# Kernel tuning notes

Measured on AMD Instinct MI355X. Metric: run time of the kernel, lower is better.

Reference implementation:

```python
import jax, jax.numpy as jnp
import numpy as np

B, N, DIM = 4, 4096, 512
H, DH, M, ITERS = 8, 64, 256, 6
KW = 33  # residual conv kernel length (along seq)


def setup_inputs() -> dict:
    key = jax.random.key(0)
    k1, k2, k3, k4 = jax.random.split(key, 4)
    return {
        "x": jax.random.normal(k1, (B, N, DIM), dtype=jnp.float32),
        "Wqkv": jax.random.normal(k2, (DIM, 3 * H * DH), dtype=jnp.float32) * 0.02,
        "Wout": jax.random.normal(k3, (H * DH, DIM), dtype=jnp.float32) * 0.02,
        "bout": jnp.zeros((DIM,), dtype=jnp.float32),
        "res_kernel": jax.random.normal(k4, (H, 1, KW, 1), dtype=jnp.float32) * 0.1,
    }


def _pinv_iter(x):
    # Moore-Penrose iterative pseudo-inverse, 6 Newton-Schulz-like steps.
    col = jnp.abs(x).sum(-1)  # ... i
    row = jnp.abs(x).sum(-2)  # ... j
    z = jnp.swapaxes(x, -1, -2) / (jnp.max(col) * jnp.max(row))
    I = jnp.eye(x.shape[-1], dtype=x.dtype)
    for _ in range(ITERS):
        xz = x @ z
        z = 0.25 * z @ (13.0 * I - xz @ (15.0 * I - xz @ (7.0 * I - xz)))
    return z


def reference(x, Wqkv, Wout, bout, res_kernel):
    b, n, _ = x.shape
    l = n // M  # landmark pooling window (n divisible by M -> no padding branch)
    scale = DH ** -0.5

    qkv = x @ Wqkv  # [b, n, 3*h*dh]
    q, k, v = jnp.split(qkv, 3, axis=-1)
    to_bhnd = lambda t: t.reshape(b, n, H, DH).transpose(0, 2, 1, 3)
    q, k, v = to_bhnd(q), to_bhnd(k), to_bhnd(v)
    q = q * scale

    # landmarks: mean over contiguous windows of size l
    q_lm = q.reshape(b, H, M, l, DH).sum(3) / l  # [b,h,m,dh]
    k_lm = k.reshape(b, H, M, l, DH).sum(3) / l

    sim1 = jnp.einsum('bhid,bhjd->bhij', q, k_lm)     # [b,h,n,m]
    sim2 = jnp.einsum('bhid,bhjd->bhij', q_lm, k_lm)  # [b,h,m,m]
    sim3 = jnp.einsum('bhid,bhjd->bhij', q_lm, k)     # [b,h,m,n]

    attn1 = jax.nn.softmax(sim1, axis=-1)
    attn2 = jax.nn.softmax(sim2, axis=-1)
    attn3 = jax.nn.softmax(sim3, axis=-1)

    attn2_inv = _pinv_iter(attn2)
    out = (attn1 @ attn2_inv) @ (attn3 @ v)  # [b,h,n,dh]

    # depthwise residual conv along the sequence axis of v
    pad = KW // 2
    conv = jax.lax.conv_general_dilated(
        v, res_kernel,
        window_strides=(1, 1),
        padding=((pad, pad), (0, 0)),
        dimension_numbers=('NCHW', 'OIHW', 'NCHW'),
        feature_group_count=H,
    )
    out = out + conv

    out = out.transpose(0, 2, 1, 3).reshape(b, n, H * DH)
    return out @ Wout + bout
```

## Files before the change

### kernel.cpp

```cpp
#include <hip/hip_runtime.h>
#include <math.h>

constexpr int BATCH = 4;
constexpr int SEQ   = 4096;
constexpr int DIMC  = 512;
constexpr int NH    = 8;
constexpr int HD    = 64;
constexpr int NLM   = 256;
constexpr int LWIN  = 16;
constexpr int KWIN  = 33;
constexpr int BH    = BATCH * NH;

typedef __attribute__((ext_vector_type(8))) short  bfrag;
typedef __attribute__((ext_vector_type(4))) float  ffrag;
typedef __attribute__((ext_vector_type(8))) unsigned short us8;
typedef __attribute__((ext_vector_type(4))) unsigned short us4;
typedef unsigned short ush;

__device__ __forceinline__ ush f2bf(float f) {
  unsigned u = __builtin_bit_cast(unsigned, f);
  return (ush)((u + 0x7FFFu + ((u >> 16) & 1u)) >> 16);
}
__device__ __forceinline__ float bf2f(ush h) {
  unsigned u = ((unsigned)h) << 16;
  return __builtin_bit_cast(float, u);
}
__device__ __forceinline__ void splitf(float f, ush& h, ush& l) {
  h = f2bf(f);
  l = f2bf(f - bf2f(h));
}
__device__ __forceinline__ void gl_lds16(const ush* g, ush* l) {
  __builtin_amdgcn_global_load_lds(
      (const __attribute__((address_space(1))) void*)g,
      (__attribute__((address_space(3))) void*)l, 16, 0, 0);
}

__global__ void split_flat(const float* __restrict__ src, ush* __restrict__ oh,
                           ush* __restrict__ ol, int n4) {
  for (int i = blockIdx.x * 256 + threadIdx.x; i < n4; i += gridDim.x * 256) {
    float4 f = ((const float4*)src)[i];
    us4 h, l;
    float fs[4] = {f.x, f.y, f.z, f.w};
#pragma unroll
    for (int j = 0; j < 4; ++j) {
      ush hh, ll;
      splitf(fs[j], hh, ll);
      h[j] = hh; l[j] = ll;
    }
    ((us4*)oh)[i] = h;
    ((us4*)ol)[i] = l;
  }
}

__global__ __launch_bounds__(256) void transpose_split_w(const float* __restrict__ in,
                                                         ush* __restrict__ oh,
                                                         ush* __restrict__ ol,
                                                         int R, int C) {
  __shared__ float T[32][33];
  const int tid = threadIdx.x;
  const int c0 = blockIdx.x * 32, r0 = blockIdx.y * 32;
#pragma unroll
  for (int u = 0; u < 4; ++u) {
    int r = (tid >> 5) * 4 + u, cl = tid & 31;
    T[r][cl] = in[(size_t)(r0 + r) * C + c0 + cl];
  }
  __syncthreads();
#pragma unroll
  for (int u = 0; u < 4; ++u) {
    int cl = (tid >> 5) * 4 + u, rl = tid & 31;
    float f = T[rl][cl];
    ush h, l; splitf(f, h, l);
    size_t o = (size_t)(c0 + cl) * R + r0 + rl;
    oh[o] = h; ol[o] = l;
  }
}

__global__ __launch_bounds__(256) void qkv_mfma(const ush* __restrict__ xh,
                                                const ush* __restrict__ xl,
                                                const ush* __restrict__ wTh,
                                                ush* __restrict__ q_bf,
                                                ush* __restrict__ k_bf,
                                                ush* __restrict__ vT,
                                                float* __restrict__ qlm,
                                                float* __restrict__ klm) {
  __shared__ ush Ash[128][40], Asl[128][40];
  __shared__ ush Bsh[128][40];
  const int tid = threadIdx.x;
  const int w = tid >> 6, lane = tid & 63;
  const int lm = lane & 15, lq = lane >> 4;
  const int wm = w >> 1, wn = w & 1;
  const int row0 = blockIdx.x * 128, col0 = blockIdx.y * 128;
  const ffrag fz = {0.f, 0.f, 0.f, 0.f};
  ffrag acc[4][4];
#pragma unroll
  for (int i = 0; i < 4; ++i)
#pragma unroll
    for (int j = 0; j < 4; ++j) acc[i][j] = fz;

  const int sm = tid >> 1, skoff = (tid & 1) * 16;
  for (int k0 = 0; k0 < 512; k0 += 32) {
    __syncthreads();
    {
      size_t ao = (size_t)(row0 + sm) * 512 + k0 + skoff;
      *(us8*)&Ash[sm][skoff]     = *(const us8*)&xh[ao];
      *(us8*)&Ash[sm][skoff + 8] = *(const us8*)&xh[ao + 8];
      *(us8*)&Asl[sm][skoff]     = *(const us8*)&xl[ao];
      *(us8*)&Asl[sm][skoff + 8] = *(const us8*)&xl[ao + 8];
      size_t bo = (size_t)(col0 + sm) * 512 + k0 + skoff;
      *(us8*)&Bsh[sm][skoff]     = *(const us8*)&wTh[bo];
      *(us8*)&Bsh[sm][skoff + 8] = *(const us8*)&wTh[bo + 8];
    }
    __syncthreads();
    bfrag ah[4], al[4], bh[4];
#pragma unroll
    for (int mt = 0; mt < 4; ++mt) {
      ah[mt] = *(const bfrag*)&Ash[64 * wm + 16 * mt + lm][8 * lq];
      al[mt] = *(const bfrag*)&Asl[64 * wm + 16 * mt + lm][8 * lq];
    }
#pragma unroll
    for (int nt = 0; nt < 4; ++nt)
      bh[nt] = *(const bfrag*)&Bsh[64 * wn + 16 * nt + lm][8 * lq];
#pragma unroll
    for (int mt = 0; mt < 4; ++mt)
#pragma unroll
      for (int nt = 0; nt < 4; ++nt) {
        acc[mt][nt] = __builtin_amdgcn_mfma_f32_16x16x32_bf16(ah[mt], bh[nt], acc[mt][nt], 0, 0, 0);
        acc[mt][nt] = __builtin_amdgcn_mfma_f32_16x16x32_bf16(al[mt], bh[nt], acc[mt][nt], 0, 0, 0);
      }
  }
#pragma unroll
  for (int mt = 0; mt < 4; ++mt) {
    int rbase = row0 + 64 * wm + 16 * mt;
    int b = rbase >> 12;
    int ntok_base = rbase & 4095;
    int win = ntok_base >> 4;
#pragma unroll
    for (int nt = 0; nt < 4; ++nt) {
      int n_local = 64 * wn + 16 * nt;
      int col = col0 + n_local + lm;
      int which = col >> 9;
      int h = (col >> 6) & 7;
      int d = col & 63;
      int bh_i = b * NH + h;
      float scale = (which == 0) ? 0.125f : 1.0f;
      float vals[4];
      float s = 0.f;
#pragma unroll
      for (int r = 0; r < 4; ++r) {
        vals[r] = acc[mt][nt][r] * scale;
        s += vals[r];
      }
      if (which == 2) {
        ush* dst = &vT[((size_t)bh_i * HD + d) * SEQ + ntok_base + 4 * lq];
#pragma unroll
        for (int r = 0; r < 4; ++r) dst[r] = f2bf(vals[r]);
      } else {
        ush* dst = which == 0 ? q_bf : k_bf;
#pragma unroll
        for (int r = 0; r < 4; ++r) {
          int ntok = ntok_base + 4 * lq + r;
          dst[((size_t)bh_i * SEQ + ntok) * HD + d] = f2bf(vals[r]);
        }
        s += __shfl_xor(s, 16);
        s += __shfl_xor(s, 32);
        if (lq == 0) {
          float* lmdst = which == 0 ? qlm : klm;
          lmdst[((size_t)bh_i * NLM + win) * HD + d] = s * (1.0f / LWIN);
        }
      }
    }
  }
}

__global__ __launch_bounds__(256) void sim2_softmax(const float* __restrict__ qlm,
                                                    const float* __restrict__ klm,
                                                    ush* __restrict__ a2h,
                                                    ush* __restrict__ a2l) {
  int i = blockIdx.x & 255;
  int bh = blockIdx.x >> 8;
  int j = threadIdx.x;
  __shared__ float qrow[64];
  __shared__ float red[256];
  if (j < 64) qrow[j] = qlm[((size_t)bh * NLM + i) * HD + j];
  __syncthreads();
  const float* kr = klm + ((size_t)bh * NLM + j) * HD;
  float s = 0.f;
#pragma unroll
  for (int d = 0; d < 64; d += 4) {
    float4 kv = *(const float4*)&kr[d];
    s += qrow[d] * kv.x + qrow[d + 1] * kv.y + qrow[d + 2] * kv.z + qrow[d + 3] * kv.w;
  }
  red[j] = s; __syncthreads();
  for (int off = 128; off > 0; off >>= 1) {
    if (j < off) red[j] = fmaxf(red[j], red[j + off]);
    __syncthreads();
  }
  float mx = red[0]; __syncthreads();
  float e = expf(s - mx);
  red[j] = e; __syncthreads();
  for (int off = 128; off > 0; off >>= 1) {
    if (j < off) red[j] += red[j + off];
    __syncthreads();
  }
  float val = e / red[0];
  size_t o = ((size_t)bh * NLM + i) * NLM + j;
  ush h, l; splitf(val, h, l);
  a2h[o] = h; a2l[o] = l;
}

__global__ __launch_bounds__(256) void colmax(const ush* __restrict__ a2h,
                                              float* __restrict__ red) {
  int bh = blockIdx.x;
  int t = threadIdx.x;
  const size_t base = (size_t)bh * NLM * NLM;
  float cs = 0.f;
  for (int i = 0; i < NLM; ++i) cs += bf2f(a2h[base + (size_t)i * NLM + t]);
  __shared__ float r1[256];
  r1[t] = cs; __syncthreads();
  for (int off = 128; off > 0; off >>= 1) {
    if (t < off) r1[t] = fmaxf(r1[t], r1[t + off]);
    __syncthreads();
  }
  if (t == 0) red[bh] = r1[0];
}

__global__ void finalize_scale(float* __restrict__ red) {
  if (threadIdx.x == 0) {
    float m1 = -1e30f;
    for (int i = 0; i < BH; ++i) m1 = fmaxf(m1, red[i]);
    red[64] = 1.0f / m1;
  }
}

__global__ __launch_bounds__(256) void zinit_split(const ush* __restrict__ a2h,
                                                   const ush* __restrict__ a2l,
                                                   const float* __restrict__ red,
                                                   ush* __restrict__ zAh, ush* __restrict__ zAl,
                                                   ush* __restrict__ zBh, ush* __restrict__ zBl) {
  __shared__ float T[32][33];
  const int tid = threadIdx.x;
  const int bh = blockIdx.z;
  const int j0 = blockIdx.x * 32, i0 = blockIdx.y * 32;
  const float s = red[64];
  const size_t base = (size_t)bh * NLM * NLM;
#pragma unroll
  for (int u = 0; u < 4; ++u) {
    int jl = (tid >> 5) * 4 + u, il = tid & 31;
    size_t o = base + (size_t)(j0 + jl) * NLM + i0 + il;
    float a = (bf2f(a2h[o]) + bf2f(a2l[o])) * s;
    T[jl][il] = a;
    ush h, l; splitf(a, h, l);
    zBh[o] = h; zBl[o] = l;
  }
  __syncthreads();
#pragma unroll
  for (int u = 0; u < 4; ++u) {
    int il = (tid >> 5) * 4 + u, jl = tid & 31;
    float a = T[jl][il];
    ush h, l; splitf(a, h, l);
    size_t o = base + (size_t)(i0 + il) * NLM + j0 + jl;
    zAh[o] = h; zAl[o] = l;
  }
}

__device__ __forceinline__ void stage_gemm(
    ush (*S)[2][8][64][8],
    const ush* Ah, const ush* Al, const ush* Bh, const ush* Bl,
    const ush* E1h, const ush* E1l, const ush* E2h, const ush* E2l,
    ush* oAh, ush* oAl, ush* oBh, ush* oBl,
    int M, int N, int K, float alpha, float beta, float coef,
    int bx, int by, int batch, int tid) {
  const size_t abase = (size_t)batch * M * K;
  const size_t bbase = (size_t)batch * N * K;
  const size_t ebase = (size_t)batch * M * N;
  const int w = tid >> 6, lane = tid & 63;
  const int lm = lane & 15, lq = lane >> 4;
  const int wm = w >> 1, wn = w & 1;
  const int row0 = bx * 64, col0 = by * 64;
  const bool uAl = (Al != nullptr);
  const bool uBl = (Bl != nullptr);
  const ffrag fz = {0.f, 0.f, 0.f, 0.f};
  ffrag acc[2][2] = {{fz, fz}, {fz, fz}};

  const size_t arow = abase + (size_t)(row0 + lane) * K;
  const size_t brow = bbase + (size_t)(col0 + lane) * K;

  for (int k0 = 0; k0 < K; k0 += 64) {
    __syncthreads();
#pragma unroll
    for (int ci = 0; ci < 2; ++ci) {
      int c = 2 * w + ci;
      gl_lds16(&Ah[arow + k0 + 8 * c], &S[0][0][c][0][0]);
      gl_lds16(&Bh[brow + k0 + 8 * c], &S[1][0][c][0][0]);
      if (uAl) gl_lds16(&Al[arow + k0 + 8 * c], &S[0][1][c][0][0]);
      if (uBl) gl_lds16(&Bl[brow + k0 + 8 * c], &S[1][1][c][0][0]);
    }
    __syncthreads();
#pragma unroll
    for (int ks = 0; ks < 2; ++ks) {
      bfrag ah[2], al[2], bhf[2], blf[2];
#pragma unroll
      for (int mt = 0; mt < 2; ++mt) {
        ah[mt] = *(const bfrag*)&S[0][0][4 * ks + lq][32 * wm + 16 * mt + lm][0];
        if (uAl) al[mt] = *(const bfrag*)&S[0][1][4 * ks + lq][32 * wm + 16 * mt + lm][0];
      }
#pragma unroll
      for (int nt = 0; nt < 2; ++nt) {
        bhf[nt] = *(const bfrag*)&S[1][0][4 * ks + lq][32 * wn + 16 * nt + lm][0];
        if (uBl) blf[nt] = *(const bfrag*)&S[1][1][4 * ks + lq][32 * wn + 16 * nt + lm][0];
      }
#pragma unroll
      for (int mt = 0; mt < 2; ++mt)
#pragma unroll
        for (int nt = 0; nt < 2; ++nt) {
          acc[mt][nt] = __builtin_amdgcn_mfma_f32_16x16x32_bf16(ah[mt], bhf[nt], acc[mt][nt], 0, 0, 0);
          if (uAl) acc[mt][nt] = __builtin_amdgcn_mfma_f32_16x16x32_bf16(al[mt], bhf[nt], acc[mt][nt], 0, 0, 0);
          if (uBl) acc[mt][nt] = __builtin_amdgcn_mfma_f32_16x16x32_bf16(ah[mt], blf[nt], acc[mt][nt], 0, 0, 0);
        }
    }
  }
#pragma unroll
  for (int mt = 0; mt < 2; ++mt)
#pragma unroll
    for (int nt = 0; nt < 2; ++nt) {
      int n = col0 + 32 * wn + 16 * nt + lm;
#pragma unroll
      for (int r = 0; r < 4; ++r) {
        int m = row0 + 32 * wm + 16 * mt + 4 * lq + r;
        float c = acc[mt][nt][r];
        float e = 0.f;
        size_t eo = ebase + (size_t)m * N + n;
        if (E1h) {
          float t = bf2f(E1h[eo]);
          if (E1l) t += bf2f(E1l[eo]);
          e += alpha * t;
        }
        if (E2h) {
          float t = bf2f(E2h[eo]);
          if (E2l) t += bf2f(E2l[eo]);
          e += beta * t;
        }
        float y = coef * (e - c);
        ush h, l; splitf(y, h, l);
        if (oAh) {
          size_t o = ebase + (size_t)m * N + n;
          oAh[o] = h;
          if (oAl) oAl[o] = l;
        }
        if (oBh) {
          size_t o = (size_t)batch * N * M + (size_t)n * M + m;
          oBh[o] = h;
          if (oBl) oBl[o] = l;
        }
      }
    }
}

__global__ __launch_bounds__(256) void bgemm_split(
    const ush* Ah, const ush* Al, const ush* Bh, const ush* Bl,
    const ush* E1h, const ush* E1l, const ush* E2h, const ush* E2l,
    ush* oAh, ush* oAl, ush* oBh, ush* oBl,
    int M, int N, int K, float alpha, float beta, float coef) {
  __shared__ ush S[2][2][8][64][8];
  stage_gemm(S, Ah, Al, Bh, Bl, E1h, E1l, E2h, E2l, oAh, oAl, oBh, oBl,
             M, N, K, alpha, beta, coef, blockIdx.x, blockIdx.y, blockIdx.z,
             threadIdx.x);
}

__global__ __launch_bounds__(256) void ns_s2(
    const ush* Yh, const ush* Yl, const ush* zh, const ush* zl,
    ush* t2h, ush* t2l, ush* Uh, ush* Ul) {
  __shared__ ush S[2][2][8][64][8];
  const int bz = blockIdx.z, batch = bz >> 1;
  if ((bz & 1) == 0) {
    stage_gemm(S, Yh, Yl, Yh, Yl, Yh, Yl, nullptr, nullptr,
               t2h, t2l, nullptr, nullptr,
               256, 256, 256, 7.f, 0.f, 1.f,
               blockIdx.x, blockIdx.y, batch, threadIdx.x);
  } else {
    stage_gemm(S, zh, zl, Yh, Yl, nullptr, nullptr, nullptr, nullptr,
               Uh, Ul, nullptr, nullptr,
               256, 256, 256, 0.f, 0.f, -1.f,
               blockIdx.x, blockIdx.y, batch, threadIdx.x);
  }
}

constexpr int NCH = 4;
__global__ __launch_bounds__(256) void sim3_mfma(const float* __restrict__ qlm,
                                                 const ush* __restrict__ k_bf,
                                                 const ush* __restrict__ vT_bf,
                                                 float* __restrict__ O_part,
                                                 float* __restrict__ l_part) {
  constexpr int CHUNK = SEQ / NCH;
  __shared__ ush Qs[64][72];
  __shared__ ush Ks[128][72];
  __shared__ ush Vs[64][136];
  __shared__ ush Ps[64][136];
  const int bh = blockIdx.z;
  const int m0 = blockIdx.x * 64;
  const int n_base = blockIdx.y * CHUNK;
  const int tid = threadIdx.x;
  const int w = tid >> 6, lane = tid & 63;
  const int lm = lane & 15, lq = lane >> 4;
  {
    int m = tid >> 2, off = (tid & 3) * 16;
    const float* src = &qlm[((size_t)bh * NLM + m0 + m) * HD + off];
    us8 o0, o1;
#pragma unroll
    for (int j = 0; j < 8; ++j) o0[j] = f2bf(src[j]);
#pragma unroll
    for (int j = 0; j < 8; ++j) o1[j] = f2bf(src[8 + j]);
    *(us8*)&Qs[m][off] = o0;
    *(us8*)&Qs[m][off + 8] = o1;
  }
  const ffrag fz = {0.f, 0.f, 0.f, 0.f};
  ffrag O[4] = {fz, fz, fz, fz};
  float lsum[4] = {0.f, 0.f, 0.f, 0.f};

  for (int n0 = 0; n0 < CHUNK; n0 += 128) {
    __syncthreads();
    {
      int n = tid >> 1, off = (tid & 1) * 32;
      const ush* src = &k_bf[((size_t)bh * SEQ + n_base + n0 + n) * HD + off];
#pragma unroll
      for (int u = 0; u < 4; ++u) *(us8*)&Ks[n][off + 8 * u] = *(const us8*)&src[8 * u];
    }
    {
      int d = tid >> 2, off = (tid & 3) * 32;
      const ush* src = &vT_bf[((size_t)bh * HD + d) * SEQ + n_base + n0 + off];
#pragma unroll
      for (int u = 0; u < 4; ++u) *(us8*)&Vs[d][off + 8 * u] = *(const us8*)&src[8 * u];
    }
    __syncthreads();
    ffrag S[8] = {fz, fz, fz, fz, fz, fz, fz, fz};
#pragma unroll
    for (int ks = 0; ks < 2; ++ks) {
      bfrag a = *(const bfrag*)&Qs[16 * w + lm][32 * ks + 8 * lq];
#pragma unroll
      for (int t = 0; t < 8; ++t) {
        bfrag b = *(const bfrag*)&Ks[16 * t + lm][32 * ks + 8 * lq];
        S[t] = __builtin_amdgcn_mfma_f32_16x16x32_bf16(a, b, S[t], 0, 0, 0);
      }
    }
#pragma unroll
    for (int t = 0; t < 8; ++t)
#pragma unroll
      for (int r = 0; r < 4; ++r) {
        float p = __expf(S[t][r]);
        lsum[r] += p;
        Ps[16 * w + 4 * lq + r][16 * t + lm] = f2bf(p);
      }
    __syncthreads();
#pragma unroll
    for (int kk = 0; kk < 4; ++kk) {
      bfrag a = *(const bfrag*)&Ps[16 * w + lm][32 * kk + 8 * lq];
#pragma unroll
      for (int t2 = 0; t2 < 4; ++t2) {
        bfrag b = *(const bfrag*)&Vs[16 * t2 + lm][32 * kk + 8 * lq];
        O[t2] = __builtin_amdgcn_mfma_f32_16x16x32_bf16(a, b, O[t2], 0, 0, 0);
      }
    }
  }
#pragma unroll
  for (int r = 0; r < 4; ++r) {
#pragma unroll
    for (int off = 1; off < 16; off <<= 1) lsum[r] += __shfl_xor(lsum[r], off);
  }
  const size_t pbase = (size_t)blockIdx.y * 32 + bh;
  if (lm == 0) {
#pragma unroll
    for (int r = 0; r < 4; ++r)
      l_part[pbase * NLM + m0 + 16 * w + 4 * lq + r] = lsum[r];
  }
#pragma unroll
  for (int t2 = 0; t2 < 4; ++t2)
#pragma unroll
    for (int r = 0; r < 4; ++r) {
      int m = m0 + 16 * w + 4 * lq + r;
      int d = 16 * t2 + lm;
      O_part[(pbase * NLM + m) * HD + d] = O[t2][r];
    }
}

__global__ __launch_bounds__(256) void sim3_finalize(const float* __restrict__ O_part,
                                                     const float* __restrict__ l_part,
                                                     ush* __restrict__ svBh,
                                                     ush* __restrict__ svBl) {
  __shared__ float T[128][17];
  __shared__ float ls[128];
  const int bh = blockIdx.y;
  const int d0 = (blockIdx.x & 3) * 16;
  const int m0 = (blockIdx.x >> 2) * 128;
  const int tid = threadIdx.x;
  if (tid < 128) {
    float s = 0.f;
#pragma unroll
    for (int c = 0; c < NCH; ++c) s += l_part[(size_t)(c * 32 + bh) * NLM + m0 + tid];
    ls[tid] = s;
  }
#pragma unroll
  for (int i = 0; i < 8; ++i) {
    int e = i * 256 + tid;
    int m = e >> 4, dd = e & 15;
    float s = 0.f;
#pragma unroll
    for (int c = 0; c < NCH; ++c)
      s += O_part[(((size_t)(c * 32 + bh)) << 14) + (size_t)(m0 + m) * HD + d0 + dd];
    T[m][dd] = s;
  }
  __syncthreads();
#pragma unroll
  for (int i = 0; i < 8; ++i) {
    int e = i * 256 + tid;
    int dd = e >> 7, m = e & 127;
    float val = T[m][dd] / ls[m];
    ush h, l; splitf(val, h, l);
    size_t o = ((size_t)bh * HD + d0 + dd) * NLM + m0 + m;
    svBh[o] = h; svBl[o] = l;
  }
}

__global__ __launch_bounds__(256) void attn1_mfma(const ush* __restrict__ q_bf,
                                                  const float* __restrict__ klm,
                                                  const ush* __restrict__ ttT,
                                                  float* __restrict__ outp) {
  __shared__ ush bufA[256 * 72];
  __shared__ ush bufB[64 * 264];
  const int bh = blockIdx.y;
  const int b = bh >> 3, h = bh & 7;
  const int i0 = blockIdx.x * 64;
  const int tid = threadIdx.x;
  const int w = tid >> 6, lane = tid & 63;
  const int lm = lane & 15, lq = lane >> 4;
  {
    int m = tid >> 2, off = (tid & 3) * 16;
    const ush* src = &q_bf[((size_t)bh * SEQ + i0 + m) * HD + off];
    *(us8*)&bufB[m * 72 + off] = *(const us8*)src;
    *(us8*)&bufB[m * 72 + off + 8] = *(const us8*)&src[8];
  }
  {
    const float* kb = klm + (size_t)bh * NLM * HD;
#pragma unroll
    for (int u = 0; u < 16; ++u) {
      int e4 = u * 256 + tid;
      float4 f = ((const float4*)kb)[e4];
      int row = e4 >> 4, col = (e4 & 15) * 4;
      ush* p = &bufA[row * 72 + col];
      p[0] = f2bf(f.x); p[1] = f2bf(f.y); p[2] = f2bf(f.z); p[3] = f2bf(f.w);
    }
  }
  __syncthreads();
  const ffrag fz = {0.f, 0.f, 0.f, 0.f};
  ffrag S[16];
#pragma unroll
  for (int t = 0; t < 16; ++t) S[t] = fz;
#pragma unroll
  for (int ks = 0; ks < 2; ++ks) {
    bfrag a = *(const bfrag*)&bufB[(16 * w + lm) * 72 + 32 * ks + 8 * lq];
#pragma unroll
    for (int t = 0; t < 16; ++t) {
      bfrag bb = *(const bfrag*)&bufA[(16 * t + lm) * 72 + 32 * ks + 8 * lq];
      S[t] = __builtin_amdgcn_mfma_f32_16x16x32_bf16(a, bb, S[t], 0, 0, 0);
    }
  }
  float rinv[4];
  float ev[16][4];
#pragma unroll
  for (int r = 0; r < 4; ++r) {
    float mx = -INFINITY;
#pragma unroll
    for (int t = 0; t < 16; ++t) mx = fmaxf(mx, S[t][r]);
#pragma unroll
    for (int off = 1; off < 16; off <<= 1) mx = fmaxf(mx, __shfl_xor(mx, off));
    float sm = 0.f;
#pragma unroll
    for (int t = 0; t < 16; ++t) { ev[t][r] = __expf(S[t][r] - mx); sm += ev[t][r]; }
#pragma unroll
    for (int off = 1; off < 16; off <<= 1) sm += __shfl_xor(sm, off);
    rinv[r] = 1.0f / sm;
  }
  __syncthreads();
#pragma unroll
  for (int t = 0; t < 16; ++t)
#pragma unroll
    for (int r = 0; r < 4; ++r)
      bufB[(16 * w + 4 * lq + r) * 264 + 16 * t + lm] = f2bf(ev[t][r]);
  {
    const ush* tb = ttT + (size_t)bh * HD * NLM;
#pragma unroll
    for (int u = 0; u < 8; ++u) {
      int e8 = u * 256 + tid;
      int row = e8 >> 5, col = (e8 & 31) * 8;
      *(us8*)&bufA[row * 264 + col] = *(const us8*)&tb[row * NLM + col];
    }
  }
  __syncthreads();
  ffrag O[4] = {fz, fz, fz, fz};
#pragma unroll
  for (int kk = 0; kk < 8; ++kk) {
    bfrag a = *(const bfrag*)&bufB[(16 * w + lm) * 264 + 32 * kk + 8 * lq];
#pragma unroll
    for (int t2 = 0; t2 < 4; ++t2) {
      bfrag bb = *(const bfrag*)&bufA[(16 * t2 + lm) * 264 + 32 * kk + 8 * lq];
      O[t2] = __builtin_amdgcn_mfma_f32_16x16x32_bf16(a, bb, O[t2], 0, 0, 0);
    }
  }
#pragma unroll
  for (int t2 = 0; t2 < 4; ++t2)
#pragma unroll
    for (int r = 0; r < 4; ++r) {
      int i = i0 + 16 * w + 4 * lq + r;
      int d = 16 * t2 + lm;
      outp[((size_t)b * SEQ + i) * DIMC + h * HD + d] = O[t2][r] * rinv[r];
    }
}

__global__ __launch_bounds__(256) void conv_add_split(const float* __restrict__ outp,
                                                      const ush* __restrict__ vT,
                                                      const float* __restrict__ kern,
                                                      ush* __restrict__ oh,
                                                      ush* __restrict__ ol) {
  __shared__ float vt[64 * 97];
  __shared__ float ks[KWIN];
  const int bh = blockIdx.y;
  const int b = bh >> 3, hh = bh & 7;
  const int n0 = blockIdx.x * 64;
  const int tid = threadIdx.x;
  if (tid < KWIN) ks[tid] = kern[hh * KWIN + tid];
  for (int e = tid; e < 64 * 96; e += 256) {
    int d = e / 96, c = e % 96;
    int n = n0 - 16 + c;
    vt[d * 97 + c] = (n >= 0 && n < SEQ) ? bf2f(vT[((size_t)bh * HD + d) * SEQ + n]) : 0.f;
  }
  __syncthreads();
  const int d = tid & 63, g = tid >> 6;
  float wreg[48];
#pragma unroll
  for (int j = 0; j < 48; ++j) wreg[j] = vt[d * 97 + g * 16 + j];
#pragma unroll
  for (int nn = 0; nn < 16; ++nn) {
    float s = 0.f;
#pragma unroll
    for (int t = 0; t < KWIN; ++t) s = fmaf(ks[t], wreg[nn + t], s);
    int n = n0 + g * 16 + nn;
    size_t o = ((size_t)b * SEQ + n) * DIMC + hh * HD + d;
    float val = outp[o] + s;
    ush h, l; splitf(val, h, l);
    oh[o] = h; ol[o] = l;
  }
}

__global__ __launch_bounds__(256) void out_gemm_split(const ush* __restrict__ ah_g,
                                                      const ush* __restrict__ al_g,
                                                      const ush* __restrict__ bh_g,
                                                      const ush* __restrict__ bl_g,
                                                      const float* __restrict__ bias,
                                                      float* __restrict__ out) {
  __shared__ ush Ash[128][40], Asl[128][40];
  __shared__ ush Bsh[128][40], Bsl[128][40];
  const int tid = threadIdx.x;
  const int w = tid >> 6, lane = tid & 63;
  const int lm = lane & 15, lq = lane >> 4;
  const int wm = w >> 1, wn = w & 1;
  const int row0 = blockIdx.x * 128, col0 = blockIdx.y * 128;
  const ffrag fz = {0.f, 0.f, 0.f, 0.f};
  ffrag acc[4][4];
#pragma unroll
  for (int i = 0; i < 4; ++i)
#pragma unroll
    for (int j = 0; j < 4; ++j) acc[i][j] = fz;

  const int sm = tid >> 1, skoff = (tid & 1) * 16;
  for (int k0 = 0; k0 < 512; k0 += 32) {
    __syncthreads();
    {
      size_t ao = (size_t)(row0 + sm) * 512 + k0 + skoff;
      *(us8*)&Ash[sm][skoff]     = *(const us8*)&ah_g[ao];
      *(us8*)&Ash[sm][skoff + 8] = *(const us8*)&ah_g[ao + 8];
      *(us8*)&Asl[sm][skoff]     = *(const us8*)&al_g[ao];
      *(us8*)&Asl[sm][skoff + 8] = *(const us8*)&al_g[ao + 8];
      size_t bo = (size_t)(col0 + sm) * 512 + k0 + skoff;
      *(us8*)&Bsh[sm][skoff]     = *(const us8*)&bh_g[bo];
      *(us8*)&Bsh[sm][skoff + 8] = *(const us8*)&bh_g[bo + 8];
      *(us8*)&Bsl[sm][skoff]     = *(const us8*)&bl_g[bo];
      *(us8*)&Bsl[sm][skoff + 8] = *(const us8*)&bl_g[bo + 8];
    }
    __syncthreads();
    bfrag ah[4], al[4], bh[4], bl[4];
#pragma unroll
    for (int mt = 0; mt < 4; ++mt) {
      ah[mt] = *(const bfrag*)&Ash[64 * wm + 16 * mt + lm][8 * lq];
      al[mt] = *(const bfrag*)&Asl[64 * wm + 16 * mt + lm][8 * lq];
    }
#pragma unroll
    for (int nt = 0; nt < 4; ++nt) {
      bh[nt] = *(const bfrag*)&Bsh[64 * wn + 16 * nt + lm][8 * lq];
      bl[nt] = *(const bfrag*)&Bsl[64 * wn + 16 * nt + lm][8 * lq];
    }
#pragma unroll
    for (int mt = 0; mt < 4; ++mt)
#pragma unroll
      for (int nt = 0; nt < 4; ++nt) {
        acc[mt][nt] = __builtin_amdgcn_mfma_f32_16x16x32_bf16(ah[mt], bh[nt], acc[mt][nt], 0, 0, 0);
        acc[mt][nt] = __builtin_amdgcn_mfma_f32_16x16x32_bf16(al[mt], bh[nt], acc[mt][nt], 0, 0, 0);
        acc[mt][nt] = __builtin_amdgcn_mfma_f32_16x16x32_bf16(ah[mt], bl[nt], acc[mt][nt], 0, 0, 0);
      }
  }
#pragma unroll
  for (int mt = 0; mt < 4; ++mt)
#pragma unroll
    for (int nt = 0; nt < 4; ++nt) {
      int n = col0 + 64 * wn + 16 * nt + lm;
      float bv = bias[n];
#pragma unroll
      for (int r = 0; r < 4; ++r) {
        int m = row0 + 64 * wm + 16 * mt + 4 * lq + r;
        out[(size_t)m * 512 + n] = acc[mt][nt][r] + bv;
      }
    }
}

extern "C" void kernel_launch(void* const* d_in, const int* in_sizes, int n_in,
                              void* d_out, int out_size, void* d_ws, size_t ws_size,
                              hipStream_t stream) {
  const float* x    = (const float*)d_in[0];
  const float* Wqkv = (const float*)d_in[1];
  const float* Wout = (const float*)d_in[2];
  const float* bout = (const float*)d_in[3];
  const float* rker = (const float*)d_in[4];
  float* out = (float*)d_out;
  float* ws = (float*)d_ws;

  ush*   vT     = (ush*)(ws);
  ush*   q_bf   = (ush*)(ws + 4194304);
  float* regA   = ws + 8388608;
  float* regB   = ws + 16777216;
  float* qlm    = ws + 25165824;
  float* klm    = ws + 25690112;
  float* regC   = ws + 26214400;
  float* a2reg  = ws + 28311552;
  float* zAreg  = ws + 30408704;
  float* zBreg  = ws + 34603008;
  float* xzreg  = ws + 38797312;
  float* t3reg  = ws + 43515904;
  float* wqkvT  = ws + 45613056;
  float* woutT  = ws + 46399488;
  float* red    = ws + 46661632;

  ush* k_bf  = (ush*)regA;
  float* outp = regA;
  ush* xh = (ush*)regB;
  ush* xl = (ush*)(regB + 4194304);
  ush* outph = (ush*)regB;
  ush* outpl = (ush*)(regB + 4194304);
  ush* a2h = (ush*)a2reg;
  ush* a2l = (ush*)(a2reg + 1048576);
  ush* zA_[4] = {(ush*)zAreg, (ush*)(zAreg + 1048576), (ush*)(zAreg + 2097152), (ush*)(zAreg + 3145728)};
  ush* zB_[4] = {(ush*)zBreg, (ush*)(zBreg + 1048576), (ush*)(zBreg + 2097152), (ush*)(zBreg + 3145728)};
  ush* Y_h  = (ush*)xzreg;
  ush* Y_l  = (ush*)(xzreg + 1048576);
  ush* t2_h = (ush*)regC;
  ush* t2_l = (ush*)(regC + 1048576);
  ush* U_h  = (ush*)t3reg;
  ush* U_l  = (ush*)(t3reg + 1048576);
  float* O_part = xzreg;
  float* l_part = xzreg + 2097152;
  ush* svB_h = (ush*)t3reg;
  ush* svB_l = (ush*)(t3reg + 262144);
  ush* ttT   = (ush*)regC;
  ush* wqkvT_h = (ush*)wqkvT;
  ush* wqkvT_l = (ush*)(wqkvT + 393216);
  ush* woutT_h = (ush*)woutT;
  ush* woutT_l = (ush*)(woutT + 131072);

  split_flat<<<2048, 256, 0, stream>>>(x, xh, xl, 2097152);
  transpose_split_w<<<dim3(48, 16), 256, 0, stream>>>(Wqkv, wqkvT_h, wqkvT_l, 512, 1536);
  transpose_split_w<<<dim3(16, 16), 256, 0, stream>>>(Wout, woutT_h, woutT_l, 512, 512);

  qkv_mfma<<<dim3(128, 12), 256, 0, stream>>>(xh, xl, wqkvT_h,
                                              q_bf, k_bf, vT, qlm, klm);

  sim2_softmax<<<8192, 256, 0, stream>>>(qlm, klm, a2h, a2l);
  colmax<<<32, 256, 0, stream>>>(a2h, red);
  finalize_scale<<<1, 64, 0, stream>>>(red);
  zinit_split<<<dim3(8, 8, 32), 256, 0, stream>>>(a2h, a2l, red,
                                                  zA_[0], zA_[1], zA_[2], zA_[3]);

  ush** zc = zA_;
  ush** zn = zB_;
  for (int it = 0; it < 6; ++it) {
    const bool zin_s  = (it == 5);
    const bool a2_s   = (it >= 4);
    const bool mid_s  = (it >= 4);
    const bool zout_s = (it >= 4);
    bgemm_split<<<dim3(4, 4, 32), 256, 0, stream>>>(
        a2h, a2_s ? a2l : nullptr,
        zc[2], zin_s ? zc[3] : nullptr,
        nullptr, nullptr, nullptr, nullptr,
        Y_h, mid_s ? Y_l : nullptr, nullptr, nullptr,
        256, 256, 256, 0.f, 0.f, -1.f);
    ns_s2<<<dim3(4, 4, 64), 256, 0, stream>>>(
        Y_h, mid_s ? Y_l : nullptr,
        zc[0], zin_s ? zc[1] : nullptr,
        t2_h, mid_s ? t2_l : nullptr,
        U_h, mid_s ? U_l : nullptr);
    bgemm_split<<<dim3(4, 4, 32), 256, 0, stream>>>(
        U_h, mid_s ? U_l : nullptr,
        t2_h, mid_s ? t2_l : nullptr,
        zc[0], zin_s ? zc[1] : nullptr,
        U_h, mid_s ? U_l : nullptr,
        zn[0], zout_s ? zn[1] : nullptr,
        zn[2], zout_s ? zn[3] : nullptr,
        256, 256, 256, -13.f, 15.f, -0.25f);
    ush** tp = zc; zc = zn; zn = tp;
  }

  sim3_mfma<<<dim3(4, NCH, 32), 256, 0, stream>>>(qlm, k_bf, vT, O_part, l_part);
  sim3_finalize<<<dim3(8, 32), 256, 0, stream>>>(O_part, l_part, svB_h, svB_l);

  bgemm_split<<<dim3(4, 1, 32), 256, 0, stream>>>(
      zc[0], zc[1], svB_h, svB_l,
      nullptr, nullptr, nullptr, nullptr,
      nullptr, nullptr, ttT, nullptr, 256, 64, 256, 0.f, 0.f, -1.f);

  attn1_mfma<<<dim3(64, 32), 256, 0, stream>>>(q_bf, klm, ttT, outp);
  conv_add_split<<<dim3(64, 32), 256, 0, stream>>>(outp, vT, rker, outph, outpl);
  out_gemm_split<<<dim3(128, 4), 256, 0, stream>>>(outph, outpl, woutT_h, woutT_l, bout, out);
}
```

Baseline: 714.2 us.

## Restructure early Newton-Schulz iterations to propagate xz and use async LDS loads in qkv

For the first four pseudo-inverse iterations, the a2·z product is no longer recomputed each step. It is updated alongside z using the identity x·z_new = -0.25·(Y·(13I - Y·(15I - Y·(7I - Y)))), with Y² saved as a side output of the t2 stage. This removes one serial GEMM launch per early iteration, so each iteration is two launches instead of three. The qkv GEMM now stages tiles with direct global-to-LDS loads in a chunked layout instead of register round-trips. The risk is that the propagated Y uses bf16-only values, so rounding error can accumulate in the early iterations.

```diff
diff --git a/kernel.cpp b/kernel.cpp
--- a/kernel.cpp
+++ b/kernel.cpp
@@ -83,8 +83,7 @@
                                                 ush* __restrict__ vT,
                                                 float* __restrict__ qlm,
                                                 float* __restrict__ klm) {
-  __shared__ ush Ash[128][40], Asl[128][40];
-  __shared__ ush Bsh[128][40];
+  __shared__ ush S[3][4][128][8];
   const int tid = threadIdx.x;
   const int w = tid >> 6, lane = tid & 63;
   const int lm = lane & 15, lq = lane >> 4;
@@ -97,29 +96,27 @@
 #pragma unroll
     for (int j = 0; j < 4; ++j) acc[i][j] = fz;
 
-  const int sm = tid >> 1, skoff = (tid & 1) * 16;
   for (int k0 = 0; k0 < 512; k0 += 32) {
     __syncthreads();
-    {
-      size_t ao = (size_t)(row0 + sm) * 512 + k0 + skoff;
-      *(us8*)&Ash[sm][skoff]     = *(const us8*)&xh[ao];
-      *(us8*)&Ash[sm][skoff + 8] = *(const us8*)&xh[ao + 8];
-      *(us8*)&Asl[sm][skoff]     = *(const us8*)&xl[ao];
-      *(us8*)&Asl[sm][skoff + 8] = *(const us8*)&xl[ao + 8];
-      size_t bo = (size_t)(col0 + sm) * 512 + k0 + skoff;
-      *(us8*)&Bsh[sm][skoff]     = *(const us8*)&wTh[bo];
-      *(us8*)&Bsh[sm][skoff + 8] = *(const us8*)&wTh[bo + 8];
+#pragma unroll
+    for (int it2 = 0; it2 < 6; ++it2) {
+      int item = 6 * w + it2;
+      int p = item >> 3, ch = (item >> 1) & 3, hf = item & 1;
+      const ush* g = (p == 0) ? xh : ((p == 1) ? xl : wTh);
+      int rb = (p == 2) ? col0 : row0;
+      gl_lds16(&g[(size_t)(rb + hf * 64 + lane) * 512 + k0 + 8 * ch],
+               &S[p][ch][hf * 64][0]);
     }
     __syncthreads();
     bfrag ah[4], al[4], bh[4];
 #pragma unroll
     for (int mt = 0; mt < 4; ++mt) {
-      ah[mt] = *(const bfrag*)&Ash[64 * wm + 16 * mt + lm][8 * lq];
-      al[mt] = *(const bfrag*)&Asl[64 * wm + 16 * mt + lm][8 * lq];
+      ah[mt] = *(const bfrag*)&S[0][lq][64 * wm + 16 * mt + lm][0];
+      al[mt] = *(const bfrag*)&S[1][lq][64 * wm + 16 * mt + lm][0];
     }
 #pragma unroll
     for (int nt = 0; nt < 4; ++nt)
-      bh[nt] = *(const bfrag*)&Bsh[64 * wn + 16 * nt + lm][8 * lq];
+      bh[nt] = *(const bfrag*)&S[2][lq][64 * wn + 16 * nt + lm][0];
 #pragma unroll
     for (int mt = 0; mt < 4; ++mt)
 #pragma unroll
@@ -267,7 +264,7 @@
     ush (*S)[2][8][64][8],
     const ush* Ah, const ush* Al, const ush* Bh, const ush* Bl,
     const ush* E1h, const ush* E1l, const ush* E2h, const ush* E2l,
-    ush* oAh, ush* oAl, ush* oBh, ush* oBl,
+    ush* oAh, ush* oAl, ush* oBh, ush* oBl, ush* oCh,
     int M, int N, int K, float alpha, float beta, float coef,
     int bx, int by, int batch, int tid) {
   const size_t abase = (size_t)batch * M * K;
@@ -352,6 +349,7 @@
           oBh[o] = h;
           if (oBl) oBl[o] = l;
         }
+        if (oCh) oCh[ebase + (size_t)m * N + n] = f2bf(c);
       }
     }
 }
@@ -363,8 +361,8 @@
     int M, int N, int K, float alpha, float beta, float coef) {
   __shared__ ush S[2][2][8][64][8];
   stage_gemm(S, Ah, Al, Bh, Bl, E1h, E1l, E2h, E2l, oAh, oAl, oBh, oBl,
-             M, N, K, alpha, beta, coef, blockIdx.x, blockIdx.y, blockIdx.z,
-             threadIdx.x);
+             nullptr, M, N, K, alpha, beta, coef,
+             blockIdx.x, blockIdx.y, blockIdx.z, threadIdx.x);
 }
 
 __global__ __launch_bounds__(256) void ns_s2(
@@ -374,13 +372,49 @@
   const int bz = blockIdx.z, batch = bz >> 1;
   if ((bz & 1) == 0) {
     stage_gemm(S, Yh, Yl, Yh, Yl, Yh, Yl, nullptr, nullptr,
-               t2h, t2l, nullptr, nullptr,
+               t2h, t2l, nullptr, nullptr, nullptr,
                256, 256, 256, 7.f, 0.f, 1.f,
                blockIdx.x, blockIdx.y, batch, threadIdx.x);
   } else {
     stage_gemm(S, zh, zl, Yh, Yl, nullptr, nullptr, nullptr, nullptr,
-               Uh, Ul, nullptr, nullptr,
+               Uh, Ul, nullptr, nullptr, nullptr,
                256, 256, 256, 0.f, 0.f, -1.f,
+               blockIdx.x, blockIdx.y, batch, threadIdx.x);
+  }
+}
+
+__global__ __launch_bounds__(256) void ns_sa(
+    const ush* Yh, const ush* zh, ush* t2h, ush* Y2h, ush* Uh) {
+  __shared__ ush S[2][2][8][64][8];
+  const int bz = blockIdx.z, batch = bz >> 1;
+  if ((bz & 1) == 0) {
+    stage_gemm(S, Yh, nullptr, Yh, nullptr, Yh, nullptr, nullptr, nullptr,
+               t2h, nullptr, nullptr, nullptr, Y2h,
+               256, 256, 256, 7.f, 0.f, 1.f,
+               blockIdx.x, blockIdx.y, batch, threadIdx.x);
+  } else {
+    stage_gemm(S, zh, nullptr, Yh, nullptr, nullptr, nullptr, nullptr, nullptr,
+               Uh, nullptr, nullptr, nullptr, nullptr,
+               256, 256, 256, 0.f, 0.f, -1.f,
+               blockIdx.x, blockIdx.y, batch, threadIdx.x);
+  }
+}
+
+__global__ __launch_bounds__(256) void ns_sb(
+    const ush* zh, const ush* Uh, const ush* t2h,
+    const ush* Yh, const ush* Y2h,
+    ush* znh, ush* znBh, ush* Ynh) {
+  __shared__ ush S[2][2][8][64][8];
+  const int bz = blockIdx.z, batch = bz >> 1;
+  if ((bz & 1) == 0) {
+    stage_gemm(S, Uh, nullptr, t2h, nullptr, zh, nullptr, Uh, nullptr,
+               znh, nullptr, znBh, nullptr, nullptr,
+               256, 256, 256, -13.f, 15.f, -0.25f,
+               blockIdx.x, blockIdx.y, batch, threadIdx.x);
+  } else {
+    stage_gemm(S, Y2h, nullptr, t2h, nullptr, Yh, nullptr, Y2h, nullptr,
+               Ynh, nullptr, nullptr, nullptr, nullptr,
+               256, 256, 256, -13.f, 15.f, -0.25f,
                blockIdx.x, blockIdx.y, batch, threadIdx.x);
   }
 }
@@ -763,6 +797,7 @@
   ush* t2_l = (ush*)(regC + 1048576);
   ush* U_h  = (ush*)t3reg;
   ush* U_l  = (ush*)(t3reg + 1048576);
+  ush* Y2_h = U_l;
   float* O_part = xzreg;
   float* l_part = xzreg + 2097152;
   ush* svB_h = (ush*)t3reg;
@@ -788,29 +823,35 @@
 
   ush** zc = zA_;
   ush** zn = zB_;
-  for (int it = 0; it < 6; ++it) {
-    const bool zin_s  = (it == 5);
-    const bool a2_s   = (it >= 4);
-    const bool mid_s  = (it >= 4);
-    const bool zout_s = (it >= 4);
+  ush* Yc = Y_h;
+  ush* Yn = Y_l;
+  bgemm_split<<<dim3(4, 4, 32), 256, 0, stream>>>(
+      a2h, nullptr, zc[2], nullptr,
+      nullptr, nullptr, nullptr, nullptr,
+      Yc, nullptr, nullptr, nullptr,
+      256, 256, 256, 0.f, 0.f, -1.f);
+  for (int it = 0; it < 4; ++it) {
+    ns_sa<<<dim3(4, 4, 64), 256, 0, stream>>>(Yc, zc[0], t2_h, Y2_h, U_h);
+    ns_sb<<<dim3(4, 4, 64), 256, 0, stream>>>(zc[0], U_h, t2_h, Yc, Y2_h,
+                                              zn[0], zn[2], Yn);
+    ush** tp = zc; zc = zn; zn = tp;
+    ush* ty = Yc; Yc = Yn; Yn = ty;
+  }
+  for (int it = 4; it < 6; ++it) {
+    const bool zin_s = (it == 5);
     bgemm_split<<<dim3(4, 4, 32), 256, 0, stream>>>(
-        a2h, a2_s ? a2l : nullptr,
-        zc[2], zin_s ? zc[3] : nullptr,
+        a2h, a2l, zc[2], zin_s ? zc[3] : nullptr,
         nullptr, nullptr, nullptr, nullptr,
-        Y_h, mid_s ? Y_l : nullptr, nullptr, nullptr,
+        Y_h, Y_l, nullptr, nullptr,
         256, 256, 256, 0.f, 0.f, -1.f);
     ns_s2<<<dim3(4, 4, 64), 256, 0, stream>>>(
-        Y_h, mid_s ? Y_l : nullptr,
+        Y_h, Y_l, zc[0], zin_s ? zc[1] : nullptr,
+        t2_h, t2_l, U_h, U_l);
+    bgemm_split<<<dim3(4, 4, 32), 256, 0, stream>>>(
+        U_h, U_l, t2_h, t2_l,
         zc[0], zin_s ? zc[1] : nullptr,
-        t2_h, mid_s ? t2_l : nullptr,
-        U_h, mid_s ? U_l : nullptr);
-    bgemm_split<<<dim3(4, 4, 32), 256, 0, stream>>>(
-        U_h, mid_s ? U_l : nullptr,
-        t2_h, mid_s ? t2_l : nullptr,
-        zc[0], zin_s ? zc[1] : nullptr,
-        U_h, mid_s ? U_l : nullptr,
-        zn[0], zout_s ? zn[1] : nullptr,
-        zn[2], zout_s ? zn[3] : nullptr,
+        U_h, U_l,
+        zn[0], zn[1], zn[2], zn[3],
         256, 256, 256, -13.f, 15.f, -0.25f);
     ush** tp = zc; zc = zn; zn = tp;
   }
```

Measured after the change: 754.8 us. 5.7% more time.
